# Performance work log

Measured on AMD Instinct MI355X. Metric: run time of the kernel, lower is better.

Reference implementation:

```python
import jax, jax.numpy as jnp
import numpy as np

CONF_THRESH = 0.9  # init kwarg confidence_thresh


def setup_inputs() -> dict:
    key = jax.random.key(0)
    k1, _ = jax.random.split(key)
    T, B, C = 2048, 64, 512
    pred = jax.random.normal(k1, (T, B, C), dtype=jnp.float32)
    mask = jnp.ones((T, B, 1), dtype=jnp.float32)
    return {"pred": pred, "mask": mask}


def reference(pred, mask):
    # pred: [T, B, C] raw scores; mask: [T, B, 1]
    C = pred.shape[-1]
    p = jax.nn.softmax(pred * mask, axis=2).reshape(-1, C)  # [N, C] probabilities
    # torch: np.where(p > thresh) selects (row, class) pairs, then
    # NLLLoss(strong_preds, classes) = mean over pairs of -p[row, class].
    sel = p > CONF_THRESH                      # [N, C] bool, selection mask
    cnt = jnp.sum(sel)                         # number of selected (row, class) pairs
    total = jnp.sum(jnp.where(sel, p, jnp.zeros((), p.dtype)))
    loss = -total / jnp.maximum(cnt, 1).astype(p.dtype)
    # if nothing passes the threshold, the original returns 0
    return jnp.where(cnt > 0, loss, jnp.zeros((), p.dtype))
```

## Files before the change

### kernel.cpp

```cpp
#include <hip/hip_runtime.h>


#define NCLS 512
#define THRESH 0.9f
#define NBLOCKS 2048
#define WAVES_PER_BLOCK 4

typedef float f32x4 __attribute__((ext_vector_type(4)));

__device__ __forceinline__ void row_reduce(f32x4 a, f32x4 b, float mval,
                                           float& wTotal, float& wCnt) {
    float x0 = a.x * mval, x1 = a.y * mval, x2 = a.z * mval, x3 = a.w * mval;
    float x4 = b.x * mval, x5 = b.y * mval, x6 = b.z * mval, x7 = b.w * mval;

    float mx = fmaxf(fmaxf(fmaxf(x0, x1), fmaxf(x2, x3)),
                     fmaxf(fmaxf(x4, x5), fmaxf(x6, x7)));
    #pragma unroll
    for (int off = 1; off < 64; off <<= 1)
        mx = fmaxf(mx, __shfl_xor(mx, off));

    float s = __expf(x0 - mx) + __expf(x1 - mx) + __expf(x2 - mx) + __expf(x3 - mx)
            + __expf(x4 - mx) + __expf(x5 - mx) + __expf(x6 - mx) + __expf(x7 - mx);
    #pragma unroll
    for (int off = 1; off < 64; off <<= 1)
        s += __shfl_xor(s, off);

    float pmax = 1.0f / s;
    if (pmax > THRESH) { wTotal += pmax; wCnt += 1.0f; }
}

__global__ __launch_bounds__(256) void pl_main(const float* __restrict__ pred,
                                               const float* __restrict__ mask,
                                               float2* __restrict__ partial,
                                               int N) {
    const int lane = threadIdx.x & 63;
    const int wid  = threadIdx.x >> 6;

    const long long nwaves = (long long)gridDim.x * WAVES_PER_BLOCK;
    const long long wave   = (long long)blockIdx.x * WAVES_PER_BLOCK + wid;
    const long long rpw    = N / nwaves;
    const long long base   = wave * rpw;
    const long long end    = base + rpw;

    float wTotal = 0.0f;
    float wCnt   = 0.0f;

    long long row = base;
    for (; row + 1 < end; row += 2) {
        const float m1 = mask[row];
        const float m2 = mask[row + 1];
        const f32x4* rp1 = (const f32x4*)(pred + row * NCLS);
        const f32x4* rp2 = (const f32x4*)(pred + (row + 1) * NCLS);
        f32x4 a1 = rp1[lane];
        f32x4 b1 = rp1[lane + 64];
        f32x4 a2 = rp2[lane];
        f32x4 b2 = rp2[lane + 64];
        row_reduce(a1, b1, m1, wTotal, wCnt);
        row_reduce(a2, b2, m2, wTotal, wCnt);
    }
    for (; row < end; ++row) {
        const float m1 = mask[row];
        const f32x4* rp1 = (const f32x4*)(pred + row * NCLS);
        f32x4 a1 = rp1[lane];
        f32x4 b1 = rp1[lane + 64];
        row_reduce(a1, b1, m1, wTotal, wCnt);
    }
    {
        long long tail = nwaves * rpw + wave;
        if (tail < (long long)N) {
            const float m1 = mask[tail];
            const f32x4* rp1 = (const f32x4*)(pred + tail * NCLS);
            f32x4 a1 = rp1[lane];
            f32x4 b1 = rp1[lane + 64];
            row_reduce(a1, b1, m1, wTotal, wCnt);
        }
    }

    __shared__ float sT[WAVES_PER_BLOCK];
    __shared__ float sC[WAVES_PER_BLOCK];
    if (lane == 0) { sT[wid] = wTotal; sC[wid] = wCnt; }
    __syncthreads();
    if (threadIdx.x == 0) {
        float t = 0.0f, c = 0.0f;
        #pragma unroll
        for (int i = 0; i < WAVES_PER_BLOCK; ++i) { t += sT[i]; c += sC[i]; }
        partial[blockIdx.x] = make_float2(t, c);
    }
}

__global__ __launch_bounds__(256) void pl_final(const float2* __restrict__ partial,
                                                int nb, float* __restrict__ out) {
    const int lane = threadIdx.x & 63;
    const int wid  = threadIdx.x >> 6;

    float t = 0.0f, c = 0.0f;
    for (int i = threadIdx.x; i < nb; i += 256) {
        float2 p = partial[i];
        t += p.x;
        c += p.y;
    }
    #pragma unroll
    for (int off = 1; off < 64; off <<= 1) {
        t += __shfl_xor(t, off);
        c += __shfl_xor(c, off);
    }
    __shared__ float sT[4];
    __shared__ float sC[4];
    if (lane == 0) { sT[wid] = t; sC[wid] = c; }
    __syncthreads();
    if (threadIdx.x == 0) {
        float tt = sT[0] + sT[1] + sT[2] + sT[3];
        float cc = sC[0] + sC[1] + sC[2] + sC[3];
        out[0] = (cc > 0.0f) ? (-tt / cc) : 0.0f;
    }
}

extern "C" void kernel_launch(void* const* d_in, const int* in_sizes, int n_in,
                              void* d_out, int out_size, void* d_ws, size_t ws_size,
                              hipStream_t stream) {
    const float* pred = (const float*)d_in[0];
    const float* mask = (const float*)d_in[1];
    float* out = (float*)d_out;
    float2* partial = (float2*)d_ws;

    const int N = in_sizes[0] / NCLS;

    pl_main<<<NBLOCKS, 256, 0, stream>>>(pred, mask, partial, N);
    pl_final<<<1, 256, 0, stream>>>(partial, NBLOCKS, out);
}
```

Before: 49.73 us.

## Fuse final reduction via last-block ticket and deepen row unrolling

Merges the two-kernel reduction into one kernel: each block publishes its partial with an atomic store, takes a ticket with an atomic add, and the last block to arrive reduces all partials and writes the result. The aim is to remove the second launch and its serialization gap. It also changes the grid to 512 blocks of 1024 threads and unrolls the row loop to four rows per iteration for more loads in flight. The ticket counter is never reset and relies on a modulo check across calls, and the ordering uses relaxed atomics plus a manual waitcnt rather than release/acquire fences, which risks reading stale partials.

```diff
diff --git a/kernel.cpp b/kernel.cpp
--- a/kernel.cpp
+++ b/kernel.cpp
@@ -3,8 +3,9 @@
 
 #define NCLS 512
 #define THRESH 0.9f
-#define NBLOCKS 2048
-#define WAVES_PER_BLOCK 4
+#define NBLOCKS 512
+#define NTHREADS 1024
+#define WAVES_PER_BLOCK 16
 
 typedef float f32x4 __attribute__((ext_vector_type(4)));
 
@@ -29,10 +30,13 @@
     if (pmax > THRESH) { wTotal += pmax; wCnt += 1.0f; }
 }
 
-__global__ __launch_bounds__(256) void pl_main(const float* __restrict__ pred,
-                                               const float* __restrict__ mask,
-                                               float2* __restrict__ partial,
-                                               int N) {
+__global__ __launch_bounds__(NTHREADS) void pl_fused(
+        const float* __restrict__ pred,
+        const float* __restrict__ mask,
+        unsigned long long* __restrict__ partial,
+        unsigned int* __restrict__ ticket,
+        float* __restrict__ out,
+        int N) {
     const int lane = threadIdx.x & 63;
     const int wid  = threadIdx.x >> 6;
 
@@ -46,17 +50,23 @@
     float wCnt   = 0.0f;
 
     long long row = base;
-    for (; row + 1 < end; row += 2) {
-        const float m1 = mask[row];
-        const float m2 = mask[row + 1];
-        const f32x4* rp1 = (const f32x4*)(pred + row * NCLS);
-        const f32x4* rp2 = (const f32x4*)(pred + (row + 1) * NCLS);
-        f32x4 a1 = rp1[lane];
-        f32x4 b1 = rp1[lane + 64];
-        f32x4 a2 = rp2[lane];
-        f32x4 b2 = rp2[lane + 64];
+    for (; row + 3 < end; row += 4) {
+        const f32x4* rp0 = (const f32x4*)(pred + (row    ) * NCLS);
+        const f32x4* rp1 = (const f32x4*)(pred + (row + 1) * NCLS);
+        const f32x4* rp2 = (const f32x4*)(pred + (row + 2) * NCLS);
+        const f32x4* rp3 = (const f32x4*)(pred + (row + 3) * NCLS);
+        const float m0 = mask[row];
+        const float m1 = mask[row + 1];
+        const float m2 = mask[row + 2];
+        const float m3 = mask[row + 3];
+        f32x4 a0 = rp0[lane], b0 = rp0[lane + 64];
+        f32x4 a1 = rp1[lane], b1 = rp1[lane + 64];
+        f32x4 a2 = rp2[lane], b2 = rp2[lane + 64];
+        f32x4 a3 = rp3[lane], b3 = rp3[lane + 64];
+        row_reduce(a0, b0, m0, wTotal, wCnt);
         row_reduce(a1, b1, m1, wTotal, wCnt);
         row_reduce(a2, b2, m2, wTotal, wCnt);
+        row_reduce(a3, b3, m3, wTotal, wCnt);
     }
     for (; row < end; ++row) {
         const float m1 = mask[row];
@@ -78,40 +88,48 @@
 
     __shared__ float sT[WAVES_PER_BLOCK];
     __shared__ float sC[WAVES_PER_BLOCK];
+    __shared__ int sLast;
     if (lane == 0) { sT[wid] = wTotal; sC[wid] = wCnt; }
     __syncthreads();
     if (threadIdx.x == 0) {
         float t = 0.0f, c = 0.0f;
         #pragma unroll
         for (int i = 0; i < WAVES_PER_BLOCK; ++i) { t += sT[i]; c += sC[i]; }
-        partial[blockIdx.x] = make_float2(t, c);
+        union { float2 f; unsigned long long u; } pub;
+        pub.f = make_float2(t, c);
+        __hip_atomic_store(&partial[blockIdx.x], pub.u, __ATOMIC_RELAXED,
+                           __HIP_MEMORY_SCOPE_AGENT);
+        asm volatile("s_waitcnt vmcnt(0)" ::: "memory");
+        unsigned int old = __hip_atomic_fetch_add(ticket, 1u, __ATOMIC_RELAXED,
+                                                  __HIP_MEMORY_SCOPE_AGENT);
+        sLast = ((old & (NBLOCKS - 1)) == (NBLOCKS - 1)) ? 1 : 0;
     }
-}
+    __syncthreads();
 
-__global__ __launch_bounds__(256) void pl_final(const float2* __restrict__ partial,
-                                                int nb, float* __restrict__ out) {
-    const int lane = threadIdx.x & 63;
-    const int wid  = threadIdx.x >> 6;
-
-    float t = 0.0f, c = 0.0f;
-    for (int i = threadIdx.x; i < nb; i += 256) {
-        float2 p = partial[i];
-        t += p.x;
-        c += p.y;
-    }
-    #pragma unroll
-    for (int off = 1; off < 64; off <<= 1) {
-        t += __shfl_xor(t, off);
-        c += __shfl_xor(c, off);
-    }
-    __shared__ float sT[4];
-    __shared__ float sC[4];
-    if (lane == 0) { sT[wid] = t; sC[wid] = c; }
-    __syncthreads();
-    if (threadIdx.x == 0) {
-        float tt = sT[0] + sT[1] + sT[2] + sT[3];
-        float cc = sC[0] + sC[1] + sC[2] + sC[3];
-        out[0] = (cc > 0.0f) ? (-tt / cc) : 0.0f;
+    if (sLast) {
+        float t = 0.0f, c = 0.0f;
+        if (threadIdx.x < NBLOCKS) {
+            union { float2 f; unsigned long long u; } got;
+            got.u = __hip_atomic_load(&partial[threadIdx.x], __ATOMIC_RELAXED,
+                                      __HIP_MEMORY_SCOPE_AGENT);
+            t = got.f.x;
+            c = got.f.y;
+        }
+        #pragma unroll
+        for (int off = 1; off < 64; off <<= 1) {
+            t += __shfl_xor(t, off);
+            c += __shfl_xor(c, off);
+        }
+        __shared__ float fT[WAVES_PER_BLOCK];
+        __shared__ float fC[WAVES_PER_BLOCK];
+        if (lane == 0) { fT[wid] = t; fC[wid] = c; }
+        __syncthreads();
+        if (threadIdx.x == 0) {
+            float tt = 0.0f, cc = 0.0f;
+            #pragma unroll
+            for (int i = 0; i < WAVES_PER_BLOCK; ++i) { tt += fT[i]; cc += fC[i]; }
+            out[0] = (cc > 0.0f) ? (-tt / cc) : 0.0f;
+        }
     }
 }
 
@@ -121,10 +139,10 @@
     const float* pred = (const float*)d_in[0];
     const float* mask = (const float*)d_in[1];
     float* out = (float*)d_out;
-    float2* partial = (float2*)d_ws;
+    unsigned long long* partial = (unsigned long long*)d_ws;
+    unsigned int* ticket = (unsigned int*)(partial + NBLOCKS);
 
     const int N = in_sizes[0] / NCLS;
 
-    pl_main<<<NBLOCKS, 256, 0, stream>>>(pred, mask, partial, N);
-    pl_final<<<1, 256, 0, stream>>>(partial, NBLOCKS, out);
+    pl_fused<<<NBLOCKS, NTHREADS, 0, stream>>>(pred, mask, partial, ticket, out, N);
 }
```

New measurement: 53.17 us. +6.9%, slower.
